# Performance work log

Hardware: AMD Instinct MI355X
Metric: run time of the kernel (lower is better)

The kernel has to match this reference:

```python
import math
import jax, jax.numpy as jnp
import numpy as np

B, N, D_IN, D_OUT = 8, 2048, 768, 768

def setup_inputs() -> dict:
    key = jax.random.key(0)
    k1, k2, k3 = jax.random.split(key, 3)
    x = jax.random.normal(k1, (B, N, D_IN), dtype=jnp.float32)
    W_qkv = jax.random.normal(k2, (D_IN, 3 * D_OUT), dtype=jnp.float32) * (1.0 / math.sqrt(D_IN))
    b_qkv = jax.random.normal(k3, (3 * D_OUT,), dtype=jnp.float32) * 0.02
    return {"x": x, "W_qkv": W_qkv, "b_qkv": b_qkv}

def reference(x, W_qkv, b_qkv):
    d_out = D_OUT
    # fused QKV projection: [B, N, 3*d_out]
    qkv = jnp.einsum('bnd,de->bne', x, W_qkv) + b_qkv
    q = qkv[:, :, :d_out]
    k = qkv[:, :, d_out:2 * d_out]
    v = qkv[:, :, 2 * d_out:3 * d_out]
    scale = 1.0 / math.sqrt(d_out)
    # scores: [B, N, N]
    scores = jnp.einsum('bqd,bkd->bqk', q, k) * scale
    attn = jax.nn.softmax(scores, axis=-1)
    # context: [B, N, d_out]
    context = jnp.einsum('bqk,bkd->bqd', attn, v)
    return context
```

## Files before the change

### kernel.cpp

```cpp
#include <hip/hip_runtime.h>
#include <hip/hip_bf16.h>

typedef __attribute__((ext_vector_type(8))) short short8;
typedef __attribute__((ext_vector_type(4))) float floatx4;

#define BATCH 8
#define SEQ 2048
#define DMODEL 768
#define NQKV 2304
#define SCALE 0.03608439182435161f

__device__ __forceinline__ ushort f2bf(float f) {
    union { float f; uint u; } in; in.f = f;
    uint u = in.u;
    return (ushort)((u + 0x7FFFu + ((u >> 16) & 1u)) >> 16);
}
__device__ __forceinline__ float bf2f(ushort h) {
    union { uint u; float f; } o; o.u = ((uint)h) << 16;
    return o.f;
}

__device__ __forceinline__ void async_copy16(void* lds_uniform, const void* gaddr) {
    __builtin_amdgcn_global_load_lds(
        (const __attribute__((address_space(1))) void*)gaddr,
        (__attribute__((address_space(3))) void*)lds_uniform,
        16, 0, 0);
}

#define BARRIER() asm volatile("s_barrier" ::: "memory")
#define LGKM0()   do { asm volatile("s_waitcnt lgkmcnt(0)" ::: "memory"); \
                       __builtin_amdgcn_sched_barrier(0); } while (0)
#define LGKM_HINT() asm volatile("s_waitcnt lgkmcnt(8)" ::: "memory")
#define VMCNT(n)  asm volatile("s_waitcnt vmcnt(" #n ")" ::: "memory")

template<int MODE, int KT>
__global__ __launch_bounds__(512, 2) void gemm8(
    const ushort* __restrict__ A, const ushort* __restrict__ B,
    const float* __restrict__ bias,
    void* __restrict__ out0, void* __restrict__ out1, void* __restrict__ out2,
    int lda, int ldb)
{
    extern __shared__ __align__(16) ushort lds[];
    const int tid  = threadIdx.x;
    const int w    = tid >> 6, lane = tid & 63;
    const int wr   = w >> 2,  wc   = w & 3;
    const int lr   = lane & 15, kg = lane >> 4;
    const int srow = lane >> 3;
    const int scc  = (lane & 7) ^ srow;

    const int m0 = blockIdx.x * 256, n0 = blockIdx.y * 256;
    const ushort* Abase;
    const ushort* Bbase;
    if (MODE == 0) {
        Abase = A + (size_t)m0 * lda;
        Bbase = B + (size_t)n0 * ldb;
    } else if (MODE == 1) {
        const int b = blockIdx.z;
        Abase = A + ((size_t)(b * SEQ + m0)) * lda;
        Bbase = B + ((size_t)(b * SEQ + n0)) * ldb;
    } else {
        const int b = blockIdx.z;
        Abase = A + (size_t)b * SEQ * SEQ + (size_t)m0 * lda;
        Bbase = B + (size_t)b * DMODEL * SEQ + (size_t)n0 * ldb;
    }

    const ushort* At[2] = { lds,         lds + 32768 };
    const ushort* Bt[2] = { lds + 16384, lds + 49152 };

    #define STG(tile, mat, half) do { if ((tile) < KT) {                          \
        ushort* sb_ = lds + (((tile) & 1) ? 32768 : 0) + ((mat) ? 16384 : 0);     \
        const ushort* g_ = (mat) ? Bbase : Abase;                                 \
        const size_t ld_ = (mat) ? (size_t)ldb : (size_t)lda;                     \
        const int k0_ = (tile) << 6;                                              \
        _Pragma("unroll")                                                         \
        for (int t_ = 0; t_ < 2; ++t_) {                                          \
            const int c8_ = (mat) ? ((w & 3) + ((w >> 2) << 3) + (t_ << 4) + ((half) << 2)) \
                                  : (w + (t_ << 4) + ((half) << 3));              \
            const int row_ = (c8_ << 3) + srow;                                   \
            async_copy16(sb_ + c8_ * 512, g_ + (size_t)row_ * ld_ + k0_ + scc * 8); \
        } } } while (0)

    short8 af[4][2], bf[4][2];
    floatx4 acc[8][4] = {};

    #define LDFRAG(tp, row, c) \
        (*reinterpret_cast<const short8*>(&(tp)[((row) << 6) + ((((c) ^ ((row) & 7))) << 3)]))

    #define READ_A(bufi, mh) do {                                                 \
        _Pragma("unroll") for (int mf_ = 0; mf_ < 4; ++mf_)                       \
        _Pragma("unroll") for (int kk_ = 0; kk_ < 2; ++kk_)                       \
            af[mf_][kk_] = LDFRAG(At[bufi], wr * 128 + ((mh) * 4 + mf_) * 16 + lr, kk_ * 4 + kg); \
    } while (0)
    #define READ_B(bufi, nh) do {                                                 \
        _Pragma("unroll") for (int nf_ = 0; nf_ < 2; ++nf_)                       \
        _Pragma("unroll") for (int kk_ = 0; kk_ < 2; ++kk_)                       \
            bf[(nh) * 2 + nf_][kk_] = LDFRAG(Bt[bufi], wc * 64 + ((nh) * 2 + nf_) * 16 + lr, kk_ * 4 + kg); \
    } while (0)
    #define MFMA_Q(mh, nh) do {                                                   \
        __builtin_amdgcn_s_setprio(1);                                            \
        _Pragma("unroll") for (int mf_ = 0; mf_ < 4; ++mf_)                       \
        _Pragma("unroll") for (int nf_ = 0; nf_ < 2; ++nf_)                       \
        _Pragma("unroll") for (int kk_ = 0; kk_ < 2; ++kk_)                       \
            acc[(mh) * 4 + mf_][(nh) * 2 + nf_] = __builtin_amdgcn_mfma_f32_16x16x32_bf16( \
                af[mf_][kk_], bf[(nh) * 2 + nf_][kk_], acc[(mh) * 4 + mf_][(nh) * 2 + nf_], 0, 0, 0); \
        __builtin_amdgcn_s_setprio(0);                                            \
    } while (0)

    STG(0, 0, 0); STG(0, 1, 0); STG(0, 1, 1); STG(0, 0, 1);
    STG(1, 0, 0); STG(1, 1, 0); STG(1, 1, 1);
    VMCNT(6);
    BARRIER();

    #pragma unroll 1
    for (int it = 0; it < KT / 2; ++it) {
        const int t = 2 * it;
        const bool lastit = (it == KT / 2 - 1);
        READ_A(0, 0); READ_B(0, 0);
        STG(t + 1, 0, 1);
        LGKM_HINT();
        BARRIER(); LGKM0();
        MFMA_Q(0, 0);
        BARRIER();
        READ_B(0, 1);
        STG(t + 2, 0, 0);
        BARRIER(); LGKM0();
        MFMA_Q(0, 1);
        BARRIER();
        READ_A(0, 1);
        STG(t + 2, 1, 0);
        BARRIER(); LGKM0();
        MFMA_Q(1, 0);
        BARRIER();
        STG(t + 2, 1, 1);
        BARRIER();
        MFMA_Q(1, 1);
        if (lastit) { VMCNT(0); } else { VMCNT(6); }
        BARRIER();
        READ_A(1, 0); READ_B(1, 0);
        STG(t + 2, 0, 1);
        LGKM_HINT();
        BARRIER(); LGKM0();
        MFMA_Q(0, 0);
        BARRIER();
        READ_B(1, 1);
        STG(t + 3, 0, 0);
        BARRIER(); LGKM0();
        MFMA_Q(0, 1);
        BARRIER();
        READ_A(1, 1);
        STG(t + 3, 1, 0);
        BARRIER(); LGKM0();
        MFMA_Q(1, 0);
        BARRIER();
        STG(t + 3, 1, 1);
        BARRIER();
        MFMA_Q(1, 1);
        VMCNT(6);
        BARRIER();
    }

    const int mrow = m0 + wr * 128;
    const int ncol = n0 + wc * 64;

    if (MODE == 0 && blockIdx.y >= 6) {
        ushort* Vt = (ushort*)out2;
        const int bIdx = m0 >> 11;
        const int ns0  = m0 & 2047;
        #pragma unroll
        for (int nf = 0; nf < 4; ++nf) {
            const int e = ncol + nf * 16 + lr;
            const int d = e - 2 * DMODEL;
            const float bv = bias[e];
            ushort* vrow = Vt + ((size_t)bIdx * DMODEL + d) * SEQ + ns0;
            #pragma unroll
            for (int a = 0; a < 8; ++a) {
                const floatx4 v = acc[a][nf];
                uint2 u;
                u.x = (uint)f2bf(v[0] + bv) | ((uint)f2bf(v[1] + bv) << 16);
                u.y = (uint)f2bf(v[2] + bv) | ((uint)f2bf(v[3] + bv) << 16);
                *reinterpret_cast<uint2*>(vrow + wr * 128 + a * 16 + kg * 4) = u;
            }
        }
    } else {
        float* scr = reinterpret_cast<float*>(reinterpret_cast<char*>(lds) + (size_t)w * 9216);
        #pragma unroll
        for (int mh = 0; mh < 2; ++mh) {
            #pragma unroll
            for (int np = 0; np < 2; ++np) {
                #pragma unroll
                for (int mf = 0; mf < 4; ++mf)
                    #pragma unroll
                    for (int nf2 = 0; nf2 < 2; ++nf2) {
                        const floatx4 v = acc[mh * 4 + mf][np * 2 + nf2];
                        #pragma unroll
                        for (int r = 0; r < 4; ++r)
                            scr[(mf * 16 + kg * 4 + r) * 36 + nf2 * 16 + lr] = v[r];
                    }
                asm volatile("s_waitcnt lgkmcnt(0)" ::: "memory");
                __builtin_amdgcn_sched_barrier(0);

                if (MODE == 2) {
                    float* Ob = (float*)out0 + (size_t)blockIdx.z * SEQ * DMODEL;
                    const int c4 = (lane & 7) * 4;
                    #pragma unroll
                    for (int p = 0; p < 8; ++p) {
                        const int row = p * 8 + (lane >> 3);
                        const float4 v = *reinterpret_cast<const float4*>(&scr[row * 36 + c4]);
                        *reinterpret_cast<float4*>(
                            &Ob[(size_t)(mrow + mh * 64 + row) * DMODEL + ncol + np * 32 + c4]) = v;
                    }
                } else {
                    const int c8 = (lane & 3) * 8;
                    const int e0 = ncol + np * 32 + c8;
                    ushort* dst; int ec; float mul;
                    float bs[8] = {0, 0, 0, 0, 0, 0, 0, 0};
                    if (MODE == 0) {
                        const bool isQ = e0 < DMODEL;
                        dst = isQ ? (ushort*)out0 : (ushort*)out1;
                        ec  = isQ ? e0 : e0 - DMODEL;
                        mul = isQ ? SCALE : 1.0f;
                        const float4 b0 = *reinterpret_cast<const float4*>(&bias[e0]);
                        const float4 b1 = *reinterpret_cast<const float4*>(&bias[e0 + 4]);
                        bs[0] = b0.x * mul; bs[1] = b0.y * mul;
                        bs[2] = b0.z * mul; bs[3] = b0.w * mul;
                        bs[4] = b1.x * mul; bs[5] = b1.y * mul;
                        bs[6] = b1.z * mul; bs[7] = b1.w * mul;
                    } else {
                        dst = (ushort*)out0 + (size_t)blockIdx.z * SEQ * SEQ;
                        ec = e0; mul = 1.0f;
                    }
                    const size_t ostride = (MODE == 0) ? (size_t)DMODEL : (size_t)SEQ;
                    #pragma unroll
                    for (int p = 0; p < 4; ++p) {
                        const int row = p * 16 + (lane >> 2);
                        const float4 lo = *reinterpret_cast<const float4*>(&scr[row * 36 + c8]);
                        const float4 hi = *reinterpret_cast<const float4*>(&scr[row * 36 + c8 + 4]);
                        short8 o;
                        o[0] = (short)f2bf(lo.x * mul + bs[0]);
                        o[1] = (short)f2bf(lo.y * mul + bs[1]);
                        o[2] = (short)f2bf(lo.z * mul + bs[2]);
                        o[3] = (short)f2bf(lo.w * mul + bs[3]);
                        o[4] = (short)f2bf(hi.x * mul + bs[4]);
                        o[5] = (short)f2bf(hi.y * mul + bs[5]);
                        o[6] = (short)f2bf(hi.z * mul + bs[6]);
                        o[7] = (short)f2bf(hi.w * mul + bs[7]);
                        *reinterpret_cast<short8*>(
                            &dst[(size_t)(mrow + mh * 64 + row) * ostride + ec]) = o;
                    }
                }
                asm volatile("s_waitcnt lgkmcnt(0)" ::: "memory");
                __builtin_amdgcn_sched_barrier(0);
            }
        }
    }
    #undef STG
    #undef LDFRAG
    #undef READ_A
    #undef READ_B
    #undef MFMA_Q
}

__global__ __launch_bounds__(256) void qkv_vtail(
    const ushort* __restrict__ Xb,
    const ushort* __restrict__ Wt,
    const float* __restrict__ bias,
    ushort* __restrict__ Vt)
{
    __shared__ __align__(16) ushort smem[2 * 128 * 32];
    ushort* As = smem;
    ushort* Bs = smem + 128 * 32;
    const int tid  = threadIdx.x;
    const int m0   = blockIdx.x * 128;
    const int n0   = 2048 + blockIdx.y * 128;
    const int wave = tid >> 6, lane = tid & 63;
    const int wm   = (wave >> 1) * 64, wn = (wave & 1) * 64;
    const int lr   = lane & 15, kg = lane >> 4;
    const ushort* Abase = Xb + (size_t)m0 * DMODEL;
    const ushort* Bbase = Wt + (size_t)n0 * DMODEL;
    floatx4 acc[4][4] = {};

    for (int k0 = 0; k0 < DMODEL; k0 += 32) {
        #pragma unroll
        for (int t = 0; t < 2; ++t) {
            const int chunk = wave * 2 + t;
            const int row = chunk * 16 + (lane >> 2);
            async_copy16(As + chunk * 512,
                         Abase + (size_t)row * DMODEL + k0 + (lane & 3) * 8);
        }
        #pragma unroll
        for (int t = 0; t < 2; ++t) {
            const int chunk = wave * 2 + t;
            const int row = chunk * 16 + (lane >> 2);
            async_copy16(Bs + chunk * 512,
                         Bbase + (size_t)row * DMODEL + k0 + (lane & 3) * 8);
        }
        __syncthreads();
        short8 a[4], b[4];
        #pragma unroll
        for (int i = 0; i < 4; ++i)
            a[i] = *reinterpret_cast<const short8*>(&As[(wm + i * 16 + lr) * 32 + kg * 8]);
        #pragma unroll
        for (int j = 0; j < 4; ++j)
            b[j] = *reinterpret_cast<const short8*>(&Bs[(wn + j * 16 + lr) * 32 + kg * 8]);
        #pragma unroll
        for (int i = 0; i < 4; ++i)
            #pragma unroll
            for (int j = 0; j < 4; ++j)
                acc[i][j] = __builtin_amdgcn_mfma_f32_16x16x32_bf16(a[i], b[j], acc[i][j], 0, 0, 0);
        __syncthreads();
    }

    const int bIdx = m0 >> 11;
    const int ns0  = m0 & 2047;
    #pragma unroll
    for (int j = 0; j < 4; ++j) {
        const int e = n0 + wn + j * 16 + lr;
        const int d = e - 2 * DMODEL;
        const float bv = bias[e];
        ushort* vrow = Vt + ((size_t)bIdx * DMODEL + d) * SEQ + ns0;
        #pragma unroll
        for (int i = 0; i < 4; ++i) {
            const floatx4 v = acc[i][j];
            uint2 u;
            u.x = (uint)f2bf(v[0] + bv) | ((uint)f2bf(v[1] + bv) << 16);
            u.y = (uint)f2bf(v[2] + bv) | ((uint)f2bf(v[3] + bv) << 16);
            *reinterpret_cast<uint2*>(vrow + wm + i * 16 + kg * 4) = u;
        }
    }
}

__global__ __launch_bounds__(256) void convert_x(const float* __restrict__ X,
                                                 ushort* __restrict__ Xb) {
    const int total = (BATCH * SEQ * DMODEL) / 8;
    for (int i = blockIdx.x * 256 + threadIdx.x; i < total; i += gridDim.x * 256) {
        const float4 v0 = reinterpret_cast<const float4*>(X)[(size_t)i * 2];
        const float4 v1 = reinterpret_cast<const float4*>(X)[(size_t)i * 2 + 1];
        uint4 u;
        u.x = (uint)f2bf(v0.x) | ((uint)f2bf(v0.y) << 16);
        u.y = (uint)f2bf(v0.z) | ((uint)f2bf(v0.w) << 16);
        u.z = (uint)f2bf(v1.x) | ((uint)f2bf(v1.y) << 16);
        u.w = (uint)f2bf(v1.z) | ((uint)f2bf(v1.w) << 16);
        reinterpret_cast<uint4*>(Xb)[i] = u;
    }
}

__global__ __launch_bounds__(256) void convert_wt(const float* __restrict__ W,
                                                  ushort* __restrict__ Wt) {
    __shared__ float tile[32][33];
    const int n0 = blockIdx.x * 32, k0 = blockIdx.y * 32;
    const int tx = threadIdx.x & 31, ty = threadIdx.x >> 5;
    #pragma unroll
    for (int i = 0; i < 32; i += 8)
        tile[ty + i][tx] = W[(size_t)(k0 + ty + i) * NQKV + n0 + tx];
    __syncthreads();
    #pragma unroll
    for (int i = 0; i < 32; i += 8)
        Wt[(size_t)(n0 + ty + i) * DMODEL + k0 + tx] = f2bf(tile[tx][ty + i]);
}

__global__ __launch_bounds__(256) void softmax_rows(ushort* __restrict__ S) {
    const int row = blockIdx.x;
    ushort* p = S + (size_t)row * SEQ;
    const int tid = threadIdx.x;
    const int wave = tid >> 6, lane = tid & 63;

    short8 v8 = *reinterpret_cast<const short8*>(p + tid * 8);
    float v[8];
    #pragma unroll
    for (int j = 0; j < 8; ++j) v[j] = bf2f((ushort)v8[j]);
    float mx = v[0];
    #pragma unroll
    for (int j = 1; j < 8; ++j) mx = fmaxf(mx, v[j]);
    #pragma unroll
    for (int off = 32; off >= 1; off >>= 1) mx = fmaxf(mx, __shfl_xor(mx, off));
    __shared__ float redm[4], reds[4];
    if (lane == 0) redm[wave] = mx;
    __syncthreads();
    mx = fmaxf(fmaxf(redm[0], redm[1]), fmaxf(redm[2], redm[3]));

    float e[8], s = 0.f;
    #pragma unroll
    for (int j = 0; j < 8; ++j) { e[j] = __expf(v[j] - mx); s += e[j]; }
    #pragma unroll
    for (int off = 32; off >= 1; off >>= 1) s += __shfl_xor(s, off);
    if (lane == 0) reds[wave] = s;
    __syncthreads();
    s = reds[0] + reds[1] + reds[2] + reds[3];
    float inv = 1.f / s;

    short8 o;
    #pragma unroll
    for (int j = 0; j < 8; ++j) o[j] = (short)f2bf(e[j] * inv);
    *reinterpret_cast<short8*>(p + tid * 8) = o;
}

extern "C" void kernel_launch(void* const* d_in, const int* in_sizes, int n_in,
                              void* d_out, int out_size, void* d_ws, size_t ws_size,
                              hipStream_t stream) {
    const float* X    = (const float*)d_in[0];
    const float* W    = (const float*)d_in[1];
    const float* bias = (const float*)d_in[2];
    float* Out = (float*)d_out;

    char* ws = (char*)d_ws;
    ushort* S  = (ushort*)ws;
    ushort* Xb = (ushort*)ws;
    ushort* Wt = (ushort*)(ws + (size_t)BATCH * SEQ * DMODEL * 2);
    ushort* Qs = (ushort*)(ws + (size_t)BATCH * SEQ * SEQ * 2);
    ushort* Kb = Qs + (size_t)BATCH * SEQ * DMODEL;
    ushort* Vt = Kb + (size_t)BATCH * SEQ * DMODEL;

    const int LDSB = 131072;
    (void)hipFuncSetAttribute((const void*)gemm8<0, 12>,
                              hipFuncAttributeMaxDynamicSharedMemorySize, LDSB);
    (void)hipFuncSetAttribute((const void*)gemm8<1, 12>,
                              hipFuncAttributeMaxDynamicSharedMemorySize, LDSB);
    (void)hipFuncSetAttribute((const void*)gemm8<2, 32>,
                              hipFuncAttributeMaxDynamicSharedMemorySize, LDSB);

    convert_x<<<2048, 256, 0, stream>>>(X, Xb);
    convert_wt<<<dim3(NQKV / 32, DMODEL / 32), 256, 0, stream>>>(W, Wt);
    gemm8<0, 12><<<dim3(64, 8), 512, LDSB, stream>>>(
        Xb, Wt, bias, Qs, Kb, Vt, DMODEL, DMODEL);
    qkv_vtail<<<dim3(128, 2), 256, 0, stream>>>(Xb, Wt, bias, Vt);
    gemm8<1, 12><<<dim3(8, 8, 8), 512, LDSB, stream>>>(
        Qs, Kb, nullptr, S, nullptr, nullptr, DMODEL, DMODEL);
    softmax_rows<<<BATCH * SEQ, 256, 0, stream>>>(S);
    gemm8<2, 32><<<dim3(8, 3, 8), 512, LDSB, stream>>>(
        S, Vt, nullptr, Out, nullptr, nullptr, SEQ, SEQ);
}
```

Baseline: 242.6 us.

## Replace PV GEMM with dedicated 128x192-tile kernel for better CU occupancy

Moves the P·V product out of the generic 256x256-tile gemm8 template into a new pv128 kernel that uses 128x192 output tiles, a grid of 16x4x8 and 80KB of LDS. The old launch produced only 192 blocks, fewer than the number of CUs. The new one launches 512 blocks, so work spreads across the GPU and more waves can be resident. The cost is lower per-block data reuse, since A and B tiles are reloaded more often, plus more global traffic for P.

```diff
diff --git a/kernel.cpp b/kernel.cpp
--- a/kernel.cpp
+++ b/kernel.cpp
@@ -54,14 +54,10 @@
     if (MODE == 0) {
         Abase = A + (size_t)m0 * lda;
         Bbase = B + (size_t)n0 * ldb;
-    } else if (MODE == 1) {
+    } else {
         const int b = blockIdx.z;
         Abase = A + ((size_t)(b * SEQ + m0)) * lda;
         Bbase = B + ((size_t)(b * SEQ + n0)) * ldb;
-    } else {
-        const int b = blockIdx.z;
-        Abase = A + (size_t)b * SEQ * SEQ + (size_t)m0 * lda;
-        Bbase = B + (size_t)b * DMODEL * SEQ + (size_t)n0 * ldb;
     }
 
     const ushort* At[2] = { lds,         lds + 32768 };
@@ -199,54 +195,42 @@
                 asm volatile("s_waitcnt lgkmcnt(0)" ::: "memory");
                 __builtin_amdgcn_sched_barrier(0);
 
-                if (MODE == 2) {
-                    float* Ob = (float*)out0 + (size_t)blockIdx.z * SEQ * DMODEL;
-                    const int c4 = (lane & 7) * 4;
-                    #pragma unroll
-                    for (int p = 0; p < 8; ++p) {
-                        const int row = p * 8 + (lane >> 3);
-                        const float4 v = *reinterpret_cast<const float4*>(&scr[row * 36 + c4]);
-                        *reinterpret_cast<float4*>(
-                            &Ob[(size_t)(mrow + mh * 64 + row) * DMODEL + ncol + np * 32 + c4]) = v;
-                    }
+                const int c8 = (lane & 3) * 8;
+                const int e0 = ncol + np * 32 + c8;
+                ushort* dst; int ec; float mul;
+                float bs[8] = {0, 0, 0, 0, 0, 0, 0, 0};
+                if (MODE == 0) {
+                    const bool isQ = e0 < DMODEL;
+                    dst = isQ ? (ushort*)out0 : (ushort*)out1;
+                    ec  = isQ ? e0 : e0 - DMODEL;
+                    mul = isQ ? SCALE : 1.0f;
+                    const float4 b0 = *reinterpret_cast<const float4*>(&bias[e0]);
+                    const float4 b1 = *reinterpret_cast<const float4*>(&bias[e0 + 4]);
+                    bs[0] = b0.x * mul; bs[1] = b0.y * mul;
+                    bs[2] = b0.z * mul; bs[3] = b0.w * mul;
+                    bs[4] = b1.x * mul; bs[5] = b1.y * mul;
+                    bs[6] = b1.z * mul; bs[7] = b1.w * mul;
                 } else {
-                    const int c8 = (lane & 3) * 8;
-                    const int e0 = ncol + np * 32 + c8;
-                    ushort* dst; int ec; float mul;
-                    float bs[8] = {0, 0, 0, 0, 0, 0, 0, 0};
-                    if (MODE == 0) {
-                        const bool isQ = e0 < DMODEL;
-                        dst = isQ ? (ushort*)out0 : (ushort*)out1;
-                        ec  = isQ ? e0 : e0 - DMODEL;
-                        mul = isQ ? SCALE : 1.0f;
-                        const float4 b0 = *reinterpret_cast<const float4*>(&bias[e0]);
-                        const float4 b1 = *reinterpret_cast<const float4*>(&bias[e0 + 4]);
-                        bs[0] = b0.x * mul; bs[1] = b0.y * mul;
-                        bs[2] = b0.z * mul; bs[3] = b0.w * mul;
-                        bs[4] = b1.x * mul; bs[5] = b1.y * mul;
-                        bs[6] = b1.z * mul; bs[7] = b1.w * mul;
-                    } else {
-                        dst = (ushort*)out0 + (size_t)blockIdx.z * SEQ * SEQ;
-                        ec = e0; mul = 1.0f;
-                    }
-                    const size_t ostride = (MODE == 0) ? (size_t)DMODEL : (size_t)SEQ;
-                    #pragma unroll
-                    for (int p = 0; p < 4; ++p) {
-                        const int row = p * 16 + (lane >> 2);
-                        const float4 lo = *reinterpret_cast<const float4*>(&scr[row * 36 + c8]);
-                        const float4 hi = *reinterpret_cast<const float4*>(&scr[row * 36 + c8 + 4]);
-                        short8 o;
-                        o[0] = (short)f2bf(lo.x * mul + bs[0]);
-                        o[1] = (short)f2bf(lo.y * mul + bs[1]);
-                        o[2] = (short)f2bf(lo.z * mul + bs[2]);
-                        o[3] = (short)f2bf(lo.w * mul + bs[3]);
-                        o[4] = (short)f2bf(hi.x * mul + bs[4]);
-                        o[5] = (short)f2bf(hi.y * mul + bs[5]);
-                        o[6] = (short)f2bf(hi.z * mul + bs[6]);
-                        o[7] = (short)f2bf(hi.w * mul + bs[7]);
-                        *reinterpret_cast<short8*>(
-                            &dst[(size_t)(mrow + mh * 64 + row) * ostride + ec]) = o;
-                    }
+                    dst = (ushort*)out0 + (size_t)blockIdx.z * SEQ * SEQ;
+                    ec = e0; mul = 1.0f;
+                }
+                const size_t ostride = (MODE == 0) ? (size_t)DMODEL : (size_t)SEQ;
+                #pragma unroll
+                for (int p = 0; p < 4; ++p) {
+                    const int row = p * 16 + (lane >> 2);
+                    const float4 lo = *reinterpret_cast<const float4*>(&scr[row * 36 + c8]);
+                    const float4 hi = *reinterpret_cast<const float4*>(&scr[row * 36 + c8 + 4]);
+                    short8 o;
+                    o[0] = (short)f2bf(lo.x * mul + bs[0]);
+                    o[1] = (short)f2bf(lo.y * mul + bs[1]);
+                    o[2] = (short)f2bf(lo.z * mul + bs[2]);
+                    o[3] = (short)f2bf(lo.w * mul + bs[3]);
+                    o[4] = (short)f2bf(hi.x * mul + bs[4]);
+                    o[5] = (short)f2bf(hi.y * mul + bs[5]);
+                    o[6] = (short)f2bf(hi.z * mul + bs[6]);
+                    o[7] = (short)f2bf(hi.w * mul + bs[7]);
+                    *reinterpret_cast<short8*>(
+                        &dst[(size_t)(mrow + mh * 64 + row) * ostride + ec]) = o;
                 }
                 asm volatile("s_waitcnt lgkmcnt(0)" ::: "memory");
                 __builtin_amdgcn_sched_barrier(0);
@@ -258,6 +242,179 @@
     #undef READ_A
     #undef READ_B
     #undef MFMA_Q
+}
+
+__global__ __launch_bounds__(512, 4) void pv128(
+    const ushort* __restrict__ P, const ushort* __restrict__ V,
+    float* __restrict__ Out)
+{
+    extern __shared__ __align__(16) ushort lds[];
+    const int tid  = threadIdx.x;
+    const int w    = tid >> 6, lane = tid & 63;
+    const int wr   = w >> 2,  wc   = w & 3;
+    const int lr   = lane & 15, kg = lane >> 4;
+    const int srow = lane >> 3;
+    const int scc  = (lane & 7) ^ srow;
+
+    const int m0 = blockIdx.x * 128, n0 = blockIdx.y * 192;
+    const int b  = blockIdx.z;
+    const ushort* Abase = P + (size_t)b * SEQ * SEQ + (size_t)m0 * SEQ;
+    const ushort* Bbase = V + (size_t)b * DMODEL * SEQ + (size_t)n0 * SEQ;
+
+    const ushort* At[2] = { lds,         lds + 8192 };
+    const ushort* Bt[2] = { lds + 16384, lds + 28672 };
+    const int KT = 32;
+
+    #define STG_A(tile, half) do { if ((tile) < KT) {                             \
+        ushort* sb_ = lds + (((tile) & 1) ? 8192 : 0);                            \
+        const int k0_ = (tile) << 6;                                              \
+        const int c8_ = (w & 3) + ((w >> 2) << 3) + ((half) << 2);                \
+        const int row_ = (c8_ << 3) + srow;                                       \
+        async_copy16(sb_ + c8_ * 512, Abase + (size_t)row_ * SEQ + k0_ + scc * 8); \
+    } } while (0)
+    #define STG_B0(tile) do { if ((tile) < KT) {                                  \
+        ushort* sb_ = lds + 16384 + (((tile) & 1) ? 12288 : 0);                   \
+        const int k0_ = (tile) << 6;                                              \
+        _Pragma("unroll")                                                         \
+        for (int t_ = 0; t_ < 2; ++t_) {                                          \
+            const int idx_ = w * 2 + t_;                                          \
+            const int c8_ = (idx_ >> 2) * 6 + (idx_ & 3);                         \
+            const int row_ = (c8_ << 3) + srow;                                   \
+            async_copy16(sb_ + c8_ * 512, Bbase + (size_t)row_ * SEQ + k0_ + scc * 8); \
+        } } } while (0)
+    #define STG_B1(tile) do { if ((tile) < KT) {                                  \
+        ushort* sb_ = lds + 16384 + (((tile) & 1) ? 12288 : 0);                   \
+        const int k0_ = (tile) << 6;                                              \
+        const int c8_ = (w >> 1) * 6 + 4 + (w & 1);                               \
+        const int row_ = (c8_ << 3) + srow;                                       \
+        async_copy16(sb_ + c8_ * 512, Bbase + (size_t)row_ * SEQ + k0_ + scc * 8); \
+    } } while (0)
+
+    short8 af[2][2], bf[3][2];
+    floatx4 acc[4][3] = {};
+
+    #define LDFRAG(tp, row, c) \
+        (*reinterpret_cast<const short8*>(&(tp)[((row) << 6) + ((((c) ^ ((row) & 7))) << 3)]))
+
+    #define READ_A(bufi, mh) do {                                                 \
+        _Pragma("unroll") for (int mf_ = 0; mf_ < 2; ++mf_)                       \
+        _Pragma("unroll") for (int kk_ = 0; kk_ < 2; ++kk_)                       \
+            af[mf_][kk_] = LDFRAG(At[bufi], wr * 64 + ((mh) * 2 + mf_) * 16 + lr, kk_ * 4 + kg); \
+    } while (0)
+    #define READ_B_N0(bufi) do {                                                  \
+        _Pragma("unroll") for (int nf_ = 0; nf_ < 2; ++nf_)                       \
+        _Pragma("unroll") for (int kk_ = 0; kk_ < 2; ++kk_)                       \
+            bf[nf_][kk_] = LDFRAG(Bt[bufi], wc * 48 + nf_ * 16 + lr, kk_ * 4 + kg); \
+    } while (0)
+    #define READ_B_N1(bufi) do {                                                  \
+        _Pragma("unroll") for (int kk_ = 0; kk_ < 2; ++kk_)                       \
+            bf[2][kk_] = LDFRAG(Bt[bufi], wc * 48 + 32 + lr, kk_ * 4 + kg);       \
+    } while (0)
+    #define MFMA_N0(mh) do {                                                      \
+        __builtin_amdgcn_s_setprio(1);                                            \
+        _Pragma("unroll") for (int mf_ = 0; mf_ < 2; ++mf_)                       \
+        _Pragma("unroll") for (int nf_ = 0; nf_ < 2; ++nf_)                       \
+        _Pragma("unroll") for (int kk_ = 0; kk_ < 2; ++kk_)                       \
+            acc[(mh) * 2 + mf_][nf_] = __builtin_amdgcn_mfma_f32_16x16x32_bf16(   \
+                af[mf_][kk_], bf[nf_][kk_], acc[(mh) * 2 + mf_][nf_], 0, 0, 0);   \
+        __builtin_amdgcn_s_setprio(0);                                            \
+    } while (0)
+    #define MFMA_N1(mh) do {                                                      \
+        __builtin_amdgcn_s_setprio(1);                                            \
+        _Pragma("unroll") for (int mf_ = 0; mf_ < 2; ++mf_)                       \
+        _Pragma("unroll") for (int kk_ = 0; kk_ < 2; ++kk_)                       \
+            acc[(mh) * 2 + mf_][2] = __builtin_amdgcn_mfma_f32_16x16x32_bf16(     \
+                af[mf_][kk_], bf[2][kk_], acc[(mh) * 2 + mf_][2], 0, 0, 0);       \
+        __builtin_amdgcn_s_setprio(0);                                            \
+    } while (0)
+
+    STG_A(0, 0); STG_B0(0); STG_B1(0); STG_A(0, 1);
+    STG_A(1, 0); STG_B0(1); STG_B1(1);
+    VMCNT(4);
+    BARRIER();
+
+    #pragma unroll 1
+    for (int it = 0; it < KT / 2; ++it) {
+        const int t = 2 * it;
+        const bool lastit = (it == KT / 2 - 1);
+        READ_A(0, 0); READ_B_N0(0);
+        STG_A(t + 1, 1);
+        BARRIER(); LGKM0();
+        MFMA_N0(0);
+        BARRIER();
+        READ_B_N1(0);
+        STG_A(t + 2, 0);
+        BARRIER(); LGKM0();
+        MFMA_N1(0);
+        BARRIER();
+        READ_A(0, 1);
+        STG_B0(t + 2);
+        BARRIER(); LGKM0();
+        MFMA_N0(1);
+        BARRIER();
+        STG_B1(t + 2);
+        BARRIER();
+        MFMA_N1(1);
+        if (lastit) { VMCNT(0); } else { VMCNT(4); }
+        BARRIER();
+        READ_A(1, 0); READ_B_N0(1);
+        STG_A(t + 2, 1);
+        BARRIER(); LGKM0();
+        MFMA_N0(0);
+        BARRIER();
+        READ_B_N1(1);
+        STG_A(t + 3, 0);
+        BARRIER(); LGKM0();
+        MFMA_N1(0);
+        BARRIER();
+        READ_A(1, 1);
+        STG_B0(t + 3);
+        BARRIER(); LGKM0();
+        MFMA_N0(1);
+        BARRIER();
+        STG_B1(t + 3);
+        BARRIER();
+        MFMA_N1(1);
+        VMCNT(4);
+        BARRIER();
+    }
+
+    const int mrow = m0 + wr * 64;
+    const int ncol = n0 + wc * 48;
+    float* scr = reinterpret_cast<float*>(reinterpret_cast<char*>(lds) + (size_t)w * 5120);
+    float* Ob = Out + (size_t)b * SEQ * DMODEL;
+    #pragma unroll
+    for (int np = 0; np < 3; ++np) {
+        #pragma unroll
+        for (int mf = 0; mf < 4; ++mf) {
+            const floatx4 v = acc[mf][np];
+            #pragma unroll
+            for (int r = 0; r < 4; ++r)
+                scr[(mf * 16 + kg * 4 + r) * 20 + lr] = v[r];
+        }
+        asm volatile("s_waitcnt lgkmcnt(0)" ::: "memory");
+        __builtin_amdgcn_sched_barrier(0);
+
+        const int c4 = (lane & 3) * 4;
+        #pragma unroll
+        for (int p = 0; p < 4; ++p) {
+            const int row = p * 16 + (lane >> 2);
+            const float4 v = *reinterpret_cast<const float4*>(&scr[row * 20 + c4]);
+            *reinterpret_cast<float4*>(
+                &Ob[(size_t)(mrow + row) * DMODEL + ncol + np * 16 + c4]) = v;
+        }
+        asm volatile("s_waitcnt lgkmcnt(0)" ::: "memory");
+        __builtin_amdgcn_sched_barrier(0);
+    }
+    #undef STG_A
+    #undef STG_B0
+    #undef STG_B1
+    #undef LDFRAG
+    #undef READ_A
+    #undef READ_B_N0
+    #undef READ_B_N1
+    #undef MFMA_N0
+    #undef MFMA_N1
 }
 
 __global__ __launch_bounds__(256) void qkv_vtail(
@@ -415,8 +572,8 @@
                               hipFuncAttributeMaxDynamicSharedMemorySize, LDSB);
     (void)hipFuncSetAttribute((const void*)gemm8<1, 12>,
                               hipFuncAttributeMaxDynamicSharedMemorySize, LDSB);
-    (void)hipFuncSetAttribute((const void*)gemm8<2, 32>,
-                              hipFuncAttributeMaxDynamicSharedMemorySize, LDSB);
+    (void)hipFuncSetAttribute((const void*)pv128,
+                              hipFuncAttributeMaxDynamicSharedMemorySize, 81920);
 
     convert_x<<<2048, 256, 0, stream>>>(X, Xb);
     convert_wt<<<dim3(NQKV / 32, DMODEL / 32), 256, 0, stream>>>(W, Wt);
@@ -426,6 +583,5 @@
     gemm8<1, 12><<<dim3(8, 8, 8), 512, LDSB, stream>>>(
         Qs, Kb, nullptr, S, nullptr, nullptr, DMODEL, DMODEL);
     softmax_rows<<<BATCH * SEQ, 256, 0, stream>>>(S);
-    gemm8<2, 32><<<dim3(8, 3, 8), 512, LDSB, stream>>>(
-        S, Vt, nullptr, Out, nullptr, nullptr, SEQ, SEQ);
-}
+    pv128<<<dim3(16, 4, 8), 512, 81920, stream>>>(S, Vt, Out);
+}
```

Result: slower. 247.6 us, median of 2 (+2.1%).
